# Kernel tuning notes

Measured on AMD Instinct MI355X. Metric: run time of the kernel, lower is better.

Reference implementation:

```python
import math
import jax, jax.numpy as jnp
import numpy as np

B, T, N, FIN, D, H, HM, L, P, O = 8, 12, 512, 3, 128, 4, 256, 3, 12, 1


def _pe(t, d):
    pos = jnp.arange(t, dtype=jnp.float32)[:, None]
    div = jnp.exp(jnp.arange(0, d, 2, dtype=jnp.float32) * (-math.log(10000.0) / d))
    pe = jnp.zeros((t, d), jnp.float32)
    pe = pe.at[:, 0::2].set(jnp.sin(pos * div))
    pe = pe.at[:, 1::2].set(jnp.cos(pos * div))
    return pe


def _spatial_attn(x, qkvW, qkvb, pW, pb):
    # attention over the node axis, per (batch, time)
    b, t, n, d = x.shape
    hd = d // H
    scale = hd ** -0.5
    qkv = jnp.einsum('btnd,ced->cbtne', x, qkvW) + qkvb[:, None, None, None, :]
    q, k, v = [a.reshape(b, t, n, H, hd) for a in qkv]
    a = jax.nn.softmax(jnp.einsum('btihe,btjhe->bthij', q, k) * scale, axis=-1)
    o = jnp.einsum('bthij,btjhe->btihe', a, v).reshape(b, t, n, d)
    return jnp.einsum('btnd,od->btno', o, pW) + pb


def _temporal_attn(x, qkvW, qkvb, pW, pb):
    # attention over the time axis, per (batch, node)
    b, t, n, d = x.shape
    hd = d // H
    scale = hd ** -0.5
    qkv = jnp.einsum('btnd,ced->cbtne', x, qkvW) + qkvb[:, None, None, None, :]
    q, k, v = [a.reshape(b, t, n, H, hd) for a in qkv]
    a = jax.nn.softmax(jnp.einsum('bxnhe,bynhe->bnhxy', q, k) * scale, axis=-1)
    o = jnp.einsum('bnhxy,bynhe->bxnhe', a, v).reshape(b, t, n, d)
    return jnp.einsum('btnd,od->btno', o, pW) + pb


def _layernorm(x, g, b, eps=1e-5):
    mu = x.mean(-1, keepdims=True)
    var = ((x - mu) ** 2).mean(-1, keepdims=True)
    return (x - mu) / jnp.sqrt(var + eps) * g + b


def setup_inputs() -> dict:
    key = jax.random.key(0)
    ks = iter(jax.random.split(key, 40))
    s = 0.02
    rn = lambda shape: jax.random.normal(next(ks), shape, jnp.float32) * s
    inp = {
        'x': jax.random.normal(next(ks), (B, T, N, FIN), jnp.float32),
        'tok_W': rn((D, FIN)), 'tok_b': rn((D,)),
        't_qkvW': rn((L, 3, D, D)), 't_qkvb': rn((L, 3, D)),
        't_pW': rn((L, D, D)), 't_pb': rn((L, D)),
        'g_qkvW': rn((L, 3, D, D)), 'g_qkvb': rn((L, 3, D)),
        'g_pW': rn((L, D, D)), 'g_pb': rn((L, D)),
        's_qkvW': rn((L, 3, D, D)), 's_qkvb': rn((L, 3, D)),
        's_pW': rn((L, D, D)), 's_pb': rn((L, D)),
        'resW': rn((L, D, D)), 'resb': rn((L, D)),
        'normW': jnp.ones((L, D), jnp.float32), 'normb': jnp.zeros((L, D), jnp.float32),
        'fc1W': rn((L, HM, 2 * D)), 'fc1b': rn((L, HM)),
        'fc2W': rn((L, D, HM)), 'fc2b': rn((L, D)),
        'end1W': rn((P, T)), 'end1b': rn((P,)),
        'end2W': rn((O, L * D)), 'end2b': rn((O,)),
    }
    return inp


def reference(x, tok_W, tok_b, t_qkvW, t_qkvb, t_pW, t_pb,
              g_qkvW, g_qkvb, g_pW, g_pb, s_qkvW, s_qkvb, s_pW, s_pb,
              resW, resb, normW, normb, fc1W, fc1b, fc2W, fc2b,
              end1W, end1b, end2W, end2b):
    # DataEmbedding: token linear + sinusoidal positional encoding over T
    h = jnp.einsum('btnf,df->btnd', x, tok_W) + tok_b
    h = h + _pe(h.shape[1], h.shape[3])[None, :, None, :]
    outs = []
    for l in range(t_qkvW.shape[0]):
        residual = h
        h = _temporal_attn(h, t_qkvW[l], t_qkvb[l], t_pW[l], t_pb[l])
        geo = _spatial_attn(h, g_qkvW[l], g_qkvb[l], g_pW[l], g_pb[l])
        sem = _spatial_attn(h, s_qkvW[l], s_qkvb[l], s_pW[l], s_pb[l])
        cat = jnp.concatenate([geo, sem], axis=-1)
        m = jax.nn.gelu(jnp.einsum('btnc,hc->btnh', cat, fc1W[l]) + fc1b[l], approximate=False)
        m = jnp.einsum('btnh,oh->btno', m, fc2W[l]) + fc2b[l]
        pre = jnp.einsum('btnd,od->btno', residual, resW[l]) + resb[l] + m
        h = _layernorm(pre, normW[l], normb[l])
        outs.append(h)
    xc = jnp.concatenate(outs, axis=-1)  # [B,T,N,L*D]
    y = jax.nn.relu(jnp.einsum('btnc,pt->bpnc', xc, end1W) + end1b[None, :, None, None])
    y = jnp.einsum('bpnc,oc->bpno', y, end2W) + end2b
    return y  # [B, pred_len, N, output_size]; structure_kl_loss is identically 0
```

## Files before the change

### kernel.cpp

```cpp
#include <hip/hip_runtime.h>
#include <hip/hip_bf16.h>
#include <math.h>

#define BB 8
#define TT 12
#define NN 512
#define FIN 3
#define DD 128
#define HH 4
#define HD 32
#define HMID 256
#define LL 3
#define PP 12
#define BTOK (TT*NN)

typedef short bf16x8 __attribute__((ext_vector_type(8)));
typedef float f32x4  __attribute__((ext_vector_type(4)));

__device__ __forceinline__ unsigned short f2bf(float f) {
    unsigned u = __float_as_uint(f);
    unsigned r = u + 0x7fffu + ((u >> 16) & 1u);
    return (unsigned short)(r >> 16);
}
__device__ __forceinline__ float bf2f(short s) {
    return __uint_as_float((unsigned)(unsigned short)s << 16);
}
__device__ __forceinline__ unsigned pk2bf(float a, float b) {
    __hip_bfloat162 h = __float22bfloat162_rn(make_float2(a, b));
    return *(unsigned*)&h;
}

__global__ __launch_bounds__(256)
void convert_weights_kernel(const float* __restrict__ t_qkvW, const float* __restrict__ t_pW,
                            const float* __restrict__ g_qkvW, const float* __restrict__ g_pW,
                            const float* __restrict__ s_qkvW, const float* __restrict__ s_pW,
                            const float* __restrict__ resW, const float* __restrict__ fc1W,
                            const float* __restrict__ fc2W, short* __restrict__ dst)
{
    int base = (blockIdx.x * 256 + threadIdx.x) * 4;
    if (base >= 933888) {
        int idx = base - 933888;
        int l = idx / 49152, r2 = idx - l*49152;
        int d = r2 / 384, col = r2 - d*384;
        const float* s2 = (col < 256) ? fc2W + ((size_t)(l*128 + d))*256 + col
                                      : resW + ((size_t)(l*128 + d))*128 + (col - 256);
        float4 v = *(const float4*)s2;
        *(uint2*)(dst + base) = make_uint2(pk2bf(v.x, v.y), pk2bf(v.z, v.w));
        return;
    }
    const float* src; int off;
    if      (base < 147456) { src = t_qkvW; off = 0; }
    else if (base < 196608) { src = t_pW;   off = 147456; }
    else if (base < 344064) { src = g_qkvW; off = 196608; }
    else if (base < 393216) { src = g_pW;   off = 344064; }
    else if (base < 540672) { src = s_qkvW; off = 393216; }
    else if (base < 589824) { src = s_pW;   off = 540672; }
    else if (base < 638976) { src = resW;   off = 589824; }
    else if (base < 835584) { src = fc1W;   off = 638976; }
    else                    { src = fc2W;   off = 835584; }
    float4 v = *(const float4*)(src + (base - off));
    *(uint2*)(dst + base) = make_uint2(pk2bf(v.x, v.y), pk2bf(v.z, v.w));
}

__global__ __launch_bounds__(256)
void combine_weights_kernel(const float* __restrict__ g_qkvW, const float* __restrict__ s_qkvW,
                            const float* __restrict__ t_pW, const float* __restrict__ g_pW,
                            const float* __restrict__ s_pW, const float* __restrict__ g_qkvb,
                            const float* __restrict__ s_qkvb, const float* __restrict__ t_pb,
                            const float* __restrict__ g_pb, const float* __restrict__ s_pb,
                            const float* __restrict__ fc1W, const float* __restrict__ fc1b,
                            short* __restrict__ wbf, float* __restrict__ qkvb2,
                            float* __restrict__ fc1b2)
{
    __shared__ float Bs[128][128];
    const int tid = threadIdx.x;
    const int blk = blockIdx.x;
    const float* A; const float* B; int arst;
    short* outp; int orst;
    int l, sel, c = 0, half = 0;
    const bool isqkv = blk < 18;
    if (isqkv) {
        l = blk / 6; int r = blk % 6; sel = r / 3; c = r % 3;
        A = (sel ? s_qkvW : g_qkvW) + (size_t)(l*3 + c) * 16384;  arst = 128;
        B = t_pW + (size_t)l * 16384;
        outp = wbf + (sel ? 393216 : 196608) + (size_t)l*49152 + (size_t)c*16384;
        orst = 128;
    } else {
        int r = blk - 18; l = r / 4; r %= 4; sel = r >> 1; half = r & 1;
        A = fc1W + (size_t)(l*256 + half*128) * 256 + sel*128;    arst = 256;
        B = (sel ? s_pW : g_pW) + (size_t)l * 16384;
        outp = wbf + 638976 + (size_t)l*65536 + (size_t)half*32768 + sel*128;
        orst = 256;
    }
    for (int idx = tid; idx < 16384; idx += 256)
        Bs[idx >> 7][idx & 127] = B[idx];
    __syncthreads();

    const int e = tid >> 1, db = (tid & 1) * 64;
    const float* Arow = A + (size_t)e * arst;
    #pragma unroll 1
    for (int ch = 0; ch < 4; ++ch) {
        float acc[16] = {};
        for (int o4 = 0; o4 < 32; ++o4) {
            float4 a4 = *(const float4*)(Arow + o4*4);
            float as[4] = {a4.x, a4.y, a4.z, a4.w};
            #pragma unroll
            for (int k = 0; k < 4; ++k) {
                #pragma unroll
                for (int j4 = 0; j4 < 4; ++j4) {
                    float4 b = *(const float4*)&Bs[o4*4 + k][db + ch*16 + j4*4];
                    acc[j4*4+0] += as[k]*b.x;
                    acc[j4*4+1] += as[k]*b.y;
                    acc[j4*4+2] += as[k]*b.z;
                    acc[j4*4+3] += as[k]*b.w;
                }
            }
        }
        short* orow = outp + (size_t)e * orst + db + ch*16;
        #pragma unroll
        for (int j = 0; j < 8; ++j)
            ((unsigned*)orow)[j] = pk2bf(acc[2*j], acc[2*j+1]);
    }

    if (tid < 128) {
        if (isqkv) {
            const float* tb = t_pb + l*128;
            const float* ar = A + (size_t)tid * 128;
            float s = (sel ? s_qkvb : g_qkvb)[(l*3 + c)*128 + tid];
            for (int o = 0; o < 128; ++o) s += ar[o] * tb[o];
            qkvb2[l*768 + sel*384 + c*128 + tid] = s;
        } else if (sel == 0) {
            int hg = half*128 + tid;
            const float* frow = fc1W + (size_t)(l*256 + hg) * 256;
            const float* gb = g_pb + l*128;
            const float* sb = s_pb + l*128;
            float s = fc1b[l*256 + hg];
            for (int o = 0; o < 128; ++o) s += frow[o]*gb[o] + frow[128+o]*sb[o];
            fc1b2[l*256 + hg] = s;
        }
    }
}

__global__ __launch_bounds__(256)
void embed_kernel(const float* __restrict__ x, const float* __restrict__ tokW,
                  const float* __restrict__ tokb, short* __restrict__ cat2)
{
    int gid = blockIdx.x * 256 + threadIdx.x;
    int d = gid & (DD - 1);
    int token = gid >> 7;
    int t = (token / NN) % TT;
    const float* xp = x + (size_t)token * FIN;
    float v = tokb[d] + xp[0]*tokW[d*3+0] + xp[1]*tokW[d*3+1] + xp[2]*tokW[d*3+2];
    int de = d & ~1;
    float freq = __expf(-(float)de * (9.210340371976184f / (float)DD));
    float ang = (float)t * freq;
    v += (d & 1) ? cosf(ang) : sinf(ang);
    cat2[(size_t)token * 384 + 256 + d] = (short)f2bf(v);
}

template<int ACT, bool OBF16>
__device__ __forceinline__ void gemm_core(
    const short* __restrict__ Ap, int lda, const short* __restrict__ W, int K,
    const float* __restrict__ bias, void* __restrict__ outp, int ldc)
{
    __shared__ __align__(16) short As[64][72];
    __shared__ __align__(16) short Bs[128][72];
    const int tid = threadIdx.x;
    const int lane = tid & 63, w = tid >> 6;
    const int wm = (w & 1) * 32, wn = (w >> 1) * 64;
    const int l15 = lane & 15, lq = lane >> 4;
    f32x4 acc[2][4] = {};
    const int arow = tid >> 2, achk = (tid & 3) * 16;
    const int brow = tid >> 1, bchk = (tid & 1) * 32;

    for (int k0 = 0; k0 < K; k0 += 64) {
        const short* ap = Ap + (size_t)arow * lda + k0 + achk;
        *(uint4*)&As[arow][achk]     = *(const uint4*)ap;
        *(uint4*)&As[arow][achk + 8] = *(const uint4*)(ap + 8);
        const short* wp = W + (size_t)brow * K + k0 + bchk;
        #pragma unroll
        for (int i = 0; i < 4; ++i)
            *(uint4*)&Bs[brow][bchk + i*8] = *(const uint4*)(wp + i*8);
        __syncthreads();
        #pragma unroll
        for (int kc = 0; kc < 2; ++kc) {
            bf16x8 af[2], bfv[4];
            #pragma unroll
            for (int mi = 0; mi < 2; ++mi)
                af[mi] = *(const bf16x8*)&As[wm + mi*16 + l15][kc*32 + lq*8];
            #pragma unroll
            for (int nj = 0; nj < 4; ++nj)
                bfv[nj] = *(const bf16x8*)&Bs[wn + nj*16 + l15][kc*32 + lq*8];
            #pragma unroll
            for (int mi = 0; mi < 2; ++mi)
                #pragma unroll
                for (int nj = 0; nj < 4; ++nj)
                    acc[mi][nj] = __builtin_amdgcn_mfma_f32_16x16x32_bf16(
                        af[mi], bfv[nj], acc[mi][nj], 0, 0, 0);
        }
        __syncthreads();
    }

    #pragma unroll
    for (int nj = 0; nj < 4; ++nj) {
        int col = wn + nj * 16 + l15;
        float bv = bias[col];
        #pragma unroll
        for (int mi = 0; mi < 2; ++mi) {
            #pragma unroll
            for (int r = 0; r < 4; ++r) {
                int row = wm + mi * 16 + lq * 4 + r;
                float v = acc[mi][nj][r] + bv;
                if (ACT == 1) v = 0.5f * v * (1.0f + erff(v * 0.7071067811865476f));
                if (OBF16) ((short*)outp)[(size_t)row * ldc + col] = (short)f2bf(v);
                else       ((float*)outp)[(size_t)row * ldc + col] = v;
            }
        }
    }
}

template<int ACT, bool OBF16>
__global__ __launch_bounds__(256)
void gemm_plain(const short* __restrict__ A, const short* __restrict__ W,
                const float* __restrict__ bias, void* __restrict__ out,
                int K, int lda, int ldc)
{
    size_t bm = (size_t)blockIdx.x * 64;
    int bn = blockIdx.y * 128;
    void* op = OBF16 ? (void*)((short*)out + bm * ldc + bn)
                     : (void*)((float*)out + bm * ldc + bn);
    gemm_core<ACT, OBF16>(A + bm * lda, lda, W + (size_t)bn * K, K, bias + bn, op, ldc);
}

__global__ __launch_bounds__(256)
void gemm_qkv_gs(const short* __restrict__ A, const short* __restrict__ W1,
                 const short* __restrict__ W2, const float* __restrict__ b1,
                 const float* __restrict__ b2, short* __restrict__ out)
{
    size_t bm = (size_t)blockIdx.x * 64;
    int y = blockIdx.y;
    const short* W = (y < 3) ? W1 : W2;
    const float* b = (y < 3) ? b1 : b2;
    int wc = ((y < 3) ? y : y - 3) * 128;
    gemm_core<0, true>(A + bm * 128, 128, W + (size_t)wc * 128, 128,
                       b + wc, out + bm * 768 + y * 128, 768);
}

__global__ __launch_bounds__(256)
void gemm_ln_kernel(const short* __restrict__ cat2, const short* __restrict__ Wc,
                    const float* __restrict__ fc2b, const float* __restrict__ resb,
                    const float* __restrict__ g, const float* __restrict__ bta,
                    short* __restrict__ cat2out, float* __restrict__ xc, int lcol)
{
    __shared__ __align__(16) short As[64][72];
    __shared__ __align__(16) short Bs[128][72];
    __shared__ float rsum[64][2], rssq[64][2];
    const int tid = threadIdx.x;
    const int lane = tid & 63, w = tid >> 6;
    const int wm = (w & 1) * 32, wn = (w >> 1) * 64;
    const int l15 = lane & 15, lq = lane >> 4;
    const size_t bm = (size_t)blockIdx.x * 64;
    f32x4 acc[2][4] = {};
    const int arow = tid >> 2, achk = (tid & 3) * 16;
    const int brow = tid >> 1, bchk = (tid & 1) * 32;
    const short* Ap = cat2 + bm * 384;

    for (int k0 = 0; k0 < 384; k0 += 64) {
        const short* ap = Ap + (size_t)arow * 384 + k0 + achk;
        *(uint4*)&As[arow][achk]     = *(const uint4*)ap;
        *(uint4*)&As[arow][achk + 8] = *(const uint4*)(ap + 8);
        const short* wp = Wc + (size_t)brow * 384 + k0 + bchk;
        #pragma unroll
        for (int i = 0; i < 4; ++i)
            *(uint4*)&Bs[brow][bchk + i*8] = *(const uint4*)(wp + i*8);
        __syncthreads();
        #pragma unroll
        for (int kc = 0; kc < 2; ++kc) {
            bf16x8 af[2], bfv[4];
            #pragma unroll
            for (int mi = 0; mi < 2; ++mi)
                af[mi] = *(const bf16x8*)&As[wm + mi*16 + l15][kc*32 + lq*8];
            #pragma unroll
            for (int nj = 0; nj < 4; ++nj)
                bfv[nj] = *(const bf16x8*)&Bs[wn + nj*16 + l15][kc*32 + lq*8];
            #pragma unroll
            for (int mi = 0; mi < 2; ++mi)
                #pragma unroll
                for (int nj = 0; nj < 4; ++nj)
                    acc[mi][nj] = __builtin_amdgcn_mfma_f32_16x16x32_bf16(
                        af[mi], bfv[nj], acc[mi][nj], 0, 0, 0);
        }
        __syncthreads();
    }

    float vv[2][4][4];
    float ps[2][4] = {}, pq[2][4] = {};
    #pragma unroll
    for (int nj = 0; nj < 4; ++nj) {
        int col = wn + nj * 16 + l15;
        float bv = fc2b[col] + resb[col];
        #pragma unroll
        for (int mi = 0; mi < 2; ++mi)
            #pragma unroll
            for (int r = 0; r < 4; ++r) {
                float v = acc[mi][nj][r] + bv;
                vv[mi][nj][r] = v;
                ps[mi][r] += v;
                pq[mi][r] += v * v;
            }
    }
    #pragma unroll
    for (int mi = 0; mi < 2; ++mi)
        #pragma unroll
        for (int r = 0; r < 4; ++r) {
            #pragma unroll
            for (int off = 1; off < 16; off <<= 1) {
                ps[mi][r] += __shfl_xor(ps[mi][r], off);
                pq[mi][r] += __shfl_xor(pq[mi][r], off);
            }
            if (l15 == 0) {
                int row = wm + mi*16 + lq*4 + r;
                rsum[row][w >> 1] = ps[mi][r];
                rssq[row][w >> 1] = pq[mi][r];
            }
        }
    __syncthreads();

    #pragma unroll
    for (int mi = 0; mi < 2; ++mi)
        #pragma unroll
        for (int r = 0; r < 4; ++r) {
            int row = wm + mi*16 + lq*4 + r;
            float s = rsum[row][0] + rsum[row][1];
            float ss = rssq[row][0] + rssq[row][1];
            float mu = s * (1.f / DD);
            float var = ss * (1.f / DD) - mu * mu;
            float rstd = rsqrtf(var + 1e-5f);
            size_t grow = bm + row;
            #pragma unroll
            for (int nj = 0; nj < 4; ++nj) {
                int col = wn + nj * 16 + l15;
                float y = (vv[mi][nj][r] - mu) * rstd * g[col] + bta[col];
                cat2out[grow * 384 + 256 + col] = (short)f2bf(y);
                xc[grow * 384 + lcol + col] = y;
            }
        }
}

__global__ __launch_bounds__(192)
void temporal_attn_kernel(const short* __restrict__ qkv, short* __restrict__ out)
{
    __shared__ __align__(16) short kvs[4][TT][264];
    const int tid = threadIdx.x;
    const int bn0 = blockIdx.x * 4;

    #pragma unroll
    for (int i = 0; i < 8; ++i) {
        int flat = (i*192 + tid) * 8;
        int ns = flat / 3072;
        int rem = flat - ns*3072;
        int t = rem >> 8, c = rem & 255;
        int bn = bn0 + ns;
        int b = bn >> 9, n = bn & (NN - 1);
        const short* src = qkv + ((size_t)(b*TT + t) * NN + n) * 384 + 128 + c;
        *(uint4*)&kvs[ns][t][c] = *(const uint4*)src;
    }

    const int nsub = tid / 48;
    const int r = tid - nsub*48;
    const int h = r / TT, ti = r - h*TT;
    const int bn = bn0 + nsub;
    const int b = bn >> 9, n = bn & (NN - 1);
    const float qscale = 0.17677669529663687f * 1.4426950408889634f;

    float q[32];
    {
        const short* qp = qkv + ((size_t)(b*TT + ti) * NN + n) * 384 + h*HD;
        #pragma unroll
        for (int i = 0; i < 16; ++i) {
            unsigned u = ((const unsigned*)qp)[i];
            q[2*i]   = __uint_as_float(u << 16) * qscale;
            q[2*i+1] = __uint_as_float(u & 0xffff0000u) * qscale;
        }
    }
    __syncthreads();

    float s[TT];
    #pragma unroll
    for (int tj = 0; tj < TT; ++tj) {
        const unsigned* kr = (const unsigned*)&kvs[nsub][tj][h*HD];
        float d0 = 0.f, d1 = 0.f;
        #pragma unroll
        for (int i = 0; i < 16; ++i) {
            unsigned u = kr[i];
            d0 += q[2*i]   * __uint_as_float(u << 16);
            d1 += q[2*i+1] * __uint_as_float(u & 0xffff0000u);
        }
        s[tj] = d0 + d1;
    }
    float sum = 0.f, p[TT];
    #pragma unroll
    for (int tj = 0; tj < TT; ++tj) { p[tj] = __builtin_amdgcn_exp2f(s[tj]); sum += p[tj]; }
    float inv = 1.f / sum;

    float o[32];
    #pragma unroll
    for (int e = 0; e < 32; ++e) o[e] = 0.f;
    #pragma unroll
    for (int tj = 0; tj < TT; ++tj) {
        const unsigned* vr = (const unsigned*)&kvs[nsub][tj][128 + h*HD];
        float pj = p[tj];
        #pragma unroll
        for (int i = 0; i < 16; ++i) {
            unsigned u = vr[i];
            o[2*i]   += pj * __uint_as_float(u << 16);
            o[2*i+1] += pj * __uint_as_float(u & 0xffff0000u);
        }
    }

    short* op = out + ((size_t)(b*TT + ti) * NN + n) * DD + h*HD;
    #pragma unroll
    for (int i = 0; i < 16; ++i)
        ((unsigned*)op)[i] = pk2bf(o[2*i] * inv, o[2*i+1] * inv);
}

__global__ __launch_bounds__(256)
void spatial_attn_mfma_kernel(const short* __restrict__ qkv, short* __restrict__ out)
{
    __shared__ __align__(16) short Qs[128][40];
    __shared__ __align__(16) short Ks[64][40];
    __shared__ __align__(16) short Vt[36][88];
    __shared__ __align__(16) short Ps[4][32][88];

    const int tid = threadIdx.x;
    const int bid = blockIdx.x;
    const int sel = bid & 1;
    const int qb = (bid >> 1) & 3;
    const int h = (bid >> 3) & 3;
    const int bt = bid >> 5;
    const int lane = tid & 63, w = tid >> 6;
    const int l15 = lane & 15, lq = lane >> 4;

    const size_t btbase = (size_t)bt * NN * 768 + sel * 384 + h * HD;
    const float qscale = 0.17677669529663687f * 1.4426950408889634f;

    {
        int r = tid >> 1, hf = (tid & 1) * 16;
        const unsigned* qp = (const unsigned*)(qkv + btbase + (size_t)(qb*128 + r) * 768 + hf);
        unsigned tmp[8];
        #pragma unroll
        for (int i = 0; i < 8; ++i) {
            unsigned u = qp[i];
            tmp[i] = pk2bf(__uint_as_float(u << 16) * qscale,
                           __uint_as_float(u & 0xffff0000u) * qscale);
        }
        *(uint4*)&Qs[r][hf]     = *(const uint4*)tmp;
        *(uint4*)&Qs[r][hf + 8] = *(const uint4*)(tmp + 4);
    }
    for (int idx = tid; idx < 4*88; idx += 256) {
        int rr = idx / 88, cc = idx - rr*88;
        Vt[32 + rr][cc] = (rr == 0 && cc < 64) ? (short)0x3F80 : (short)0;
    }

    f32x4 acc_o[2][3] = {};
    const int ve = tid & 31, vkb = (tid >> 5) * 8;

    for (int kt = 0; kt < 8; ++kt) {
        __syncthreads();
        {
            int r = tid >> 2, c = (tid & 3) * 8;
            const short* kp = qkv + btbase + (size_t)(kt*64 + r) * 768 + 128 + c;
            *(uint4*)&Ks[r][c] = *(const uint4*)kp;
        }
        {
            const short* vp = qkv + btbase + (size_t)(kt*64 + vkb) * 768 + 256 + ve;
            short tmp[8];
            #pragma unroll
            for (int jj = 0; jj < 8; ++jj) tmp[jj] = vp[(size_t)jj * 768];
            *(uint4*)&Vt[ve][vkb] = *(const uint4*)tmp;
        }
        __syncthreads();

        bf16x8 kf[4], qf[2];
        #pragma unroll
        for (int km = 0; km < 4; ++km)
            kf[km] = *(const bf16x8*)&Ks[km*16 + l15][lq*8];
        #pragma unroll
        for (int qn = 0; qn < 2; ++qn)
            qf[qn] = *(const bf16x8*)&Qs[w*32 + qn*16 + l15][lq*8];
        f32x4 sacc[4][2] = {};
        #pragma unroll
        for (int km = 0; km < 4; ++km)
            #pragma unroll
            for (int qn = 0; qn < 2; ++qn)
                sacc[km][qn] = __builtin_amdgcn_mfma_f32_16x16x32_bf16(
                    kf[km], qf[qn], sacc[km][qn], 0, 0, 0);

        #pragma unroll
        for (int km = 0; km < 4; ++km)
            #pragma unroll
            for (int qn = 0; qn < 2; ++qn) {
                float e0 = __builtin_amdgcn_exp2f(sacc[km][qn][0]);
                float e1 = __builtin_amdgcn_exp2f(sacc[km][qn][1]);
                float e2 = __builtin_amdgcn_exp2f(sacc[km][qn][2]);
                float e3 = __builtin_amdgcn_exp2f(sacc[km][qn][3]);
                *(uint2*)&Ps[w][qn*16 + l15][km*16 + lq*4] =
                    make_uint2(pk2bf(e0, e1), pk2bf(e2, e3));
            }

        #pragma unroll
        for (int kk = 0; kk < 2; ++kk) {
            bf16x8 pa[2], vb[3];
            #pragma unroll
            for (int mi = 0; mi < 2; ++mi)
                pa[mi] = *(const bf16x8*)&Ps[w][mi*16 + l15][kk*32 + lq*8];
            #pragma unroll
            for (int nj = 0; nj < 3; ++nj)
                vb[nj] = *(const bf16x8*)&Vt[nj*16 + l15][kk*32 + lq*8];
            #pragma unroll
            for (int mi = 0; mi < 2; ++mi)
                #pragma unroll
                for (int nj = 0; nj < 3; ++nj)
                    acc_o[mi][nj] = __builtin_amdgcn_mfma_f32_16x16x32_bf16(
                        pa[mi], vb[nj], acc_o[mi][nj], 0, 0, 0);
        }
    }

    #pragma unroll
    for (int mi = 0; mi < 2; ++mi) {
        #pragma unroll
        for (int r = 0; r < 4; ++r) {
            float l = __shfl(acc_o[mi][2][r], lane & 48);
            float inv = 1.f / l;
            int qrow = qb*128 + w*32 + mi*16 + lq*4 + r;
            short* op = out + ((size_t)bt * NN + qrow) * 256 + sel*128 + h*HD;
            op[l15]      = (short)f2bf(acc_o[mi][0][r] * inv);
            op[16 + l15] = (short)f2bf(acc_o[mi][1][r] * inv);
        }
    }
}

__global__ __launch_bounds__(256)
void head_kernel(const float* __restrict__ xc, const float* __restrict__ e1W,
                 const float* __restrict__ e1b, const float* __restrict__ e2W,
                 const float* __restrict__ e2b, float* __restrict__ out)
{
    __shared__ float xcs[TT][LL*DD];
    __shared__ float w1[PP*TT];
    int bid = blockIdx.x;
    int b = bid >> 9, n = bid & (NN - 1);
    int tid = threadIdx.x;
    if (tid < PP*TT) w1[tid] = e1W[tid];
    #pragma unroll
    for (int i = 0; i < 18; ++i) {
        int f = i*256 + tid;
        int t = f / (LL*DD), c = f % (LL*DD);
        xcs[t][c] = xc[(((size_t)(b*TT + t) * NN) + n) * (LL*DD) + c];
    }
    __syncthreads();
    int p = tid >> 4, lane16 = tid & 15;
    float acc = 0.f;
    if (p < PP) {
        for (int c = lane16; c < LL*DD; c += 16) {
            float tmp = e1b[p];
            #pragma unroll
            for (int t = 0; t < TT; ++t) tmp += xcs[t][c] * w1[p*TT + t];
            tmp = fmaxf(tmp, 0.f);
            acc += tmp * e2W[c];
        }
    }
    acc += __shfl_xor(acc, 1);
    acc += __shfl_xor(acc, 2);
    acc += __shfl_xor(acc, 4);
    acc += __shfl_xor(acc, 8);
    if (p < PP && lane16 == 0)
        out[((size_t)(b*PP + p)) * NN + n] = acc + e2b[0];
}

extern "C" void kernel_launch(void* const* d_in, const int* in_sizes, int n_in,
                              void* d_out, int out_size, void* d_ws, size_t ws_size,
                              hipStream_t stream)
{
    const float* x      = (const float*)d_in[0];
    const float* tok_W  = (const float*)d_in[1];
    const float* tok_b  = (const float*)d_in[2];
    const float* t_qkvW = (const float*)d_in[3];
    const float* t_qkvb = (const float*)d_in[4];
    const float* t_pW   = (const float*)d_in[5];
    const float* t_pb   = (const float*)d_in[6];
    const float* g_qkvW = (const float*)d_in[7];
    const float* g_qkvb = (const float*)d_in[8];
    const float* g_pW   = (const float*)d_in[9];
    const float* g_pb   = (const float*)d_in[10];
    const float* s_qkvW = (const float*)d_in[11];
    const float* s_qkvb = (const float*)d_in[12];
    const float* s_pW   = (const float*)d_in[13];
    const float* s_pb   = (const float*)d_in[14];
    const float* resW   = (const float*)d_in[15];
    const float* resb   = (const float*)d_in[16];
    const float* normW  = (const float*)d_in[17];
    const float* normb  = (const float*)d_in[18];
    const float* fc1W   = (const float*)d_in[19];
    const float* fc1b   = (const float*)d_in[20];
    const float* fc2W   = (const float*)d_in[21];
    const float* fc2b   = (const float*)d_in[22];
    const float* end1W  = (const float*)d_in[23];
    const float* end1b  = (const float*)d_in[24];
    const float* end2W  = (const float*)d_in[25];
    const float* end2b  = (const float*)d_in[26];
    float* out = (float*)d_out;

    short* wbf = (short*)d_ws;
    const size_t WBF = 1081344;
    float* qkvb2 = (float*)(wbf + WBF);
    float* fc1b2 = qkvb2 + 2304;
    short* act   = (short*)(fc1b2 + 768);

    convert_weights_kernel<<<1056, 256, 0, stream>>>(
        t_qkvW, t_pW, g_qkvW, g_pW, s_qkvW, s_pW, resW, fc1W, fc2W, wbf);
    combine_weights_kernel<<<30, 256, 0, stream>>>(
        g_qkvW, s_qkvW, t_pW, g_pW, s_pW, g_qkvb, s_qkvb, t_pb, g_pb, s_pb,
        fc1W, fc1b, wbf, qkvb2, fc1b2);

    const size_t fixedBytes = WBF*2 + 3072*4;
    const size_t perBatchBytes = (size_t)BTOK * 4352;
    int nb = 8;
    while (nb > 1 && fixedBytes + (size_t)nb * perBatchBytes > ws_size) nb >>= 1;

    for (int b0 = 0; b0 < BB; b0 += nb) {
        const int CT = nb * BTOK;
        const int GM = CT / 64;
        short* cat2 = act;
        short* qkvh = cat2 + (size_t)CT*384;
        short* atmp = qkvh + (size_t)CT*768;
        float* xc   = (float*)(atmp + (size_t)CT*256);

        const float* xch = x + (size_t)b0 * BTOK * FIN;
        float* outch = out + (size_t)b0 * PP * NN;

        embed_kernel<<<CT*DD/256, 256, 0, stream>>>(xch, tok_W, tok_b, cat2);

        for (int l = 0; l < LL; ++l) {
            const short* tqw = wbf + 0      + (size_t)l*49152;
            const short* gqw = wbf + 196608 + (size_t)l*49152;
            const short* sqw = wbf + 393216 + (size_t)l*49152;
            const short* f1w = wbf + 638976 + (size_t)l*65536;
            const short* f2rw= wbf + 933888 + (size_t)l*49152;
            const float* tqb = t_qkvb + (size_t)l*384;

            gemm_plain<0,true><<<dim3(GM,3), 256, 0, stream>>>(
                cat2 + 256, tqw, tqb, qkvh, 128, 384, 384);
            temporal_attn_kernel<<<nb*NN/4, 192, 0, stream>>>(qkvh, atmp);

            gemm_qkv_gs<<<dim3(GM,6), 256, 0, stream>>>(
                atmp, gqw, sqw, qkvb2 + l*768, qkvb2 + l*768 + 384, qkvh);
            spatial_attn_mfma_kernel<<<nb*TT*HH*4*2, 256, 0, stream>>>(qkvh, atmp);

            gemm_plain<1,true><<<dim3(GM,2), 256, 0, stream>>>(
                atmp, f1w, fc1b2 + l*256, cat2, 256, 256, 384);
            gemm_ln_kernel<<<GM, 256, 0, stream>>>(
                cat2, f2rw, fc2b + (size_t)l*128, resb + (size_t)l*128,
                normW + (size_t)l*128, normb + (size_t)l*128, cat2, xc, l*DD);
        }

        head_kernel<<<nb*NN, 256, 0, stream>>>(xc, end1W, end1b, end2W, end2b, outch);
    }
}
```

Baseline: 716.1 us.

## Store spatial QKV in head-major planes for contiguous attention loads

The spatial QKV projection now writes each (branch, head, q/k/v) slice into its own contiguous plane of 32-element rows instead of a 768-wide interleaved row. The spatial attention kernel reads Q, K and V from these planes, so K and V tile loads touch contiguous memory rather than striding by 768 elements. LDS padding for Vt and Ps also shrinks from 88 to 72. The GEMM epilogue now does scattered scalar stores into the planes, which may cost write efficiency, and the narrower padding could change bank-conflict behavior.

```diff
diff --git a/kernel.cpp b/kernel.cpp
--- a/kernel.cpp
+++ b/kernel.cpp
@@ -235,15 +235,69 @@
 __global__ __launch_bounds__(256)
 void gemm_qkv_gs(const short* __restrict__ A, const short* __restrict__ W1,
                  const short* __restrict__ W2, const float* __restrict__ b1,
-                 const float* __restrict__ b2, short* __restrict__ out)
-{
-    size_t bm = (size_t)blockIdx.x * 64;
-    int y = blockIdx.y;
-    const short* W = (y < 3) ? W1 : W2;
-    const float* b = (y < 3) ? b1 : b2;
-    int wc = ((y < 3) ? y : y - 3) * 128;
-    gemm_core<0, true>(A + bm * 128, 128, W + (size_t)wc * 128, 128,
-                       b + wc, out + bm * 768 + y * 128, 768);
+                 const float* __restrict__ b2, short* __restrict__ out, int CT)
+{
+    __shared__ __align__(16) short As[64][72];
+    __shared__ __align__(16) short Bs[128][72];
+    const int tid = threadIdx.x;
+    const int lane = tid & 63, w = tid >> 6;
+    const int wm = (w & 1) * 32, wn = (w >> 1) * 64;
+    const int l15 = lane & 15, lq = lane >> 4;
+    const size_t bm = (size_t)blockIdx.x * 64;
+    const int y = blockIdx.y;
+    const int sel = (y < 3) ? 0 : 1;
+    const int comp = (y < 3) ? y : y - 3;
+    const short* W = (sel ? W2 : W1) + (size_t)comp * 128 * 128;
+    const float* bias = (sel ? b2 : b1) + comp * 128;
+    const short* Ap = A + bm * 128;
+    f32x4 acc[2][4] = {};
+    const int arow = tid >> 2, achk = (tid & 3) * 16;
+    const int brow = tid >> 1, bchk = (tid & 1) * 32;
+
+    for (int k0 = 0; k0 < 128; k0 += 64) {
+        const short* ap = Ap + (size_t)arow * 128 + k0 + achk;
+        *(uint4*)&As[arow][achk]     = *(const uint4*)ap;
+        *(uint4*)&As[arow][achk + 8] = *(const uint4*)(ap + 8);
+        const short* wp = W + (size_t)brow * 128 + k0 + bchk;
+        #pragma unroll
+        for (int i = 0; i < 4; ++i)
+            *(uint4*)&Bs[brow][bchk + i*8] = *(const uint4*)(wp + i*8);
+        __syncthreads();
+        #pragma unroll
+        for (int kc = 0; kc < 2; ++kc) {
+            bf16x8 af[2], bfv[4];
+            #pragma unroll
+            for (int mi = 0; mi < 2; ++mi)
+                af[mi] = *(const bf16x8*)&As[wm + mi*16 + l15][kc*32 + lq*8];
+            #pragma unroll
+            for (int nj = 0; nj < 4; ++nj)
+                bfv[nj] = *(const bf16x8*)&Bs[wn + nj*16 + l15][kc*32 + lq*8];
+            #pragma unroll
+            for (int mi = 0; mi < 2; ++mi)
+                #pragma unroll
+                for (int nj = 0; nj < 4; ++nj)
+                    acc[mi][nj] = __builtin_amdgcn_mfma_f32_16x16x32_bf16(
+                        af[mi], bfv[nj], acc[mi][nj], 0, 0, 0);
+        }
+        __syncthreads();
+    }
+
+    #pragma unroll
+    for (int nj = 0; nj < 4; ++nj) {
+        int col16 = wn + nj * 16;
+        int h = col16 >> 5;
+        int e0 = (col16 & 16) + l15;
+        float bv = bias[col16 + l15];
+        short* plane = out + ((size_t)((sel*4 + h)*3 + comp) * CT) * 32;
+        #pragma unroll
+        for (int mi = 0; mi < 2; ++mi) {
+            #pragma unroll
+            for (int r = 0; r < 4; ++r) {
+                size_t row = bm + wm + mi * 16 + lq * 4 + r;
+                plane[row * 32 + e0] = (short)f2bf(acc[mi][nj][r] + bv);
+            }
+        }
+    }
 }
 
 __global__ __launch_bounds__(256)
@@ -425,12 +479,13 @@
 }
 
 __global__ __launch_bounds__(256)
-void spatial_attn_mfma_kernel(const short* __restrict__ qkv, short* __restrict__ out)
+void spatial_attn_mfma_kernel(const short* __restrict__ qkv, short* __restrict__ out,
+                              int CT)
 {
     __shared__ __align__(16) short Qs[128][40];
     __shared__ __align__(16) short Ks[64][40];
-    __shared__ __align__(16) short Vt[36][88];
-    __shared__ __align__(16) short Ps[4][32][88];
+    __shared__ __align__(16) short Vt[36][72];
+    __shared__ __align__(16) short Ps[4][32][72];
 
     const int tid = threadIdx.x;
     const int bid = blockIdx.x;
@@ -441,12 +496,15 @@
     const int lane = tid & 63, w = tid >> 6;
     const int l15 = lane & 15, lq = lane >> 4;
 
-    const size_t btbase = (size_t)bt * NN * 768 + sel * 384 + h * HD;
+    const short* qpl = qkv + ((size_t)((sel*4 + h)*3 + 0) * CT) * 32;
+    const short* kpl = qpl + (size_t)CT * 32;
+    const short* vpl = kpl + (size_t)CT * 32;
+    const int tokbase = bt * NN;
     const float qscale = 0.17677669529663687f * 1.4426950408889634f;
 
     {
         int r = tid >> 1, hf = (tid & 1) * 16;
-        const unsigned* qp = (const unsigned*)(qkv + btbase + (size_t)(qb*128 + r) * 768 + hf);
+        const unsigned* qp = (const unsigned*)(qpl + (size_t)(tokbase + qb*128 + r) * 32 + hf);
         unsigned tmp[8];
         #pragma unroll
         for (int i = 0; i < 8; ++i) {
@@ -457,8 +515,8 @@
         *(uint4*)&Qs[r][hf]     = *(const uint4*)tmp;
         *(uint4*)&Qs[r][hf + 8] = *(const uint4*)(tmp + 4);
     }
-    for (int idx = tid; idx < 4*88; idx += 256) {
-        int rr = idx / 88, cc = idx - rr*88;
+    for (int idx = tid; idx < 4*72; idx += 256) {
+        int rr = idx / 72, cc = idx - rr*72;
         Vt[32 + rr][cc] = (rr == 0 && cc < 64) ? (short)0x3F80 : (short)0;
     }
 
@@ -469,14 +527,14 @@
         __syncthreads();
         {
             int r = tid >> 2, c = (tid & 3) * 8;
-            const short* kp = qkv + btbase + (size_t)(kt*64 + r) * 768 + 128 + c;
+            const short* kp = kpl + (size_t)(tokbase + kt*64 + r) * 32 + c;
             *(uint4*)&Ks[r][c] = *(const uint4*)kp;
         }
         {
-            const short* vp = qkv + btbase + (size_t)(kt*64 + vkb) * 768 + 256 + ve;
+            const short* vp = vpl + (size_t)(tokbase + kt*64 + vkb) * 32 + ve;
             short tmp[8];
             #pragma unroll
-            for (int jj = 0; jj < 8; ++jj) tmp[jj] = vp[(size_t)jj * 768];
+            for (int jj = 0; jj < 8; ++jj) tmp[jj] = vp[(size_t)jj * 32];
             *(uint4*)&Vt[ve][vkb] = *(const uint4*)tmp;
         }
         __syncthreads();
@@ -533,7 +591,7 @@
             float l = __shfl(acc_o[mi][2][r], lane & 48);
             float inv = 1.f / l;
             int qrow = qb*128 + w*32 + mi*16 + lq*4 + r;
-            short* op = out + ((size_t)bt * NN + qrow) * 256 + sel*128 + h*HD;
+            short* op = out + ((size_t)tokbase + qrow) * 256 + sel*128 + h*HD;
             op[l15]      = (short)f2bf(acc_o[mi][0][r] * inv);
             op[16 + l15] = (short)f2bf(acc_o[mi][1][r] * inv);
         }
@@ -653,8 +711,8 @@
             temporal_attn_kernel<<<nb*NN/4, 192, 0, stream>>>(qkvh, atmp);
 
             gemm_qkv_gs<<<dim3(GM,6), 256, 0, stream>>>(
-                atmp, gqw, sqw, qkvb2 + l*768, qkvb2 + l*768 + 384, qkvh);
-            spatial_attn_mfma_kernel<<<nb*TT*HH*4*2, 256, 0, stream>>>(qkvh, atmp);
+                atmp, gqw, sqw, qkvb2 + l*768, qkvb2 + l*768 + 384, qkvh, CT);
+            spatial_attn_mfma_kernel<<<nb*TT*HH*4*2, 256, 0, stream>>>(qkvh, atmp, CT);
 
             gemm_plain<1,true><<<dim3(GM,2), 256, 0, stream>>>(
                 atmp, f1w, fc1b2 + l*256, cat2, 256, 256, 384);
```

Result: faster. 697.4 us (-2.6%).
